# Kernel tuning notes

Hardware: AMD Instinct MI355X
Metric: run time of the kernel (lower is better)

Reference implementation:

```python
import jax, jax.numpy as jnp
import numpy as np

FORGET_BIAS = 1.0  # TF LSTMCell default

def _lstm_step(c, h, x, W, b):
    # TF BasicLSTM/LSTMCell gate order: i, j (cell candidate), f, o
    z = jnp.concatenate([x, h], axis=-1) @ W + b
    i, j, f, o = jnp.split(z, 4, axis=-1)
    c_new = c * jax.nn.sigmoid(f + FORGET_BIAS) + jax.nn.sigmoid(i) * jnp.tanh(j)
    h_new = jnp.tanh(c_new) * jax.nn.sigmoid(o)
    return c_new, h_new

def setup_inputs() -> dict:
    key = jax.random.key(0)
    k1, k2, k3 = jax.random.split(key, 3)
    B, T, D, H1, H2 = 512, 2048, 1, 64, 1
    x = jax.random.normal(k1, (B, T, D), dtype=jnp.float32)
    W1 = jax.random.normal(k2, (D + H1, 4 * H1), dtype=jnp.float32) * 0.1
    b1 = jnp.zeros((4 * H1,), dtype=jnp.float32)
    W2 = jax.random.normal(k3, (H1 + H2, 4 * H2), dtype=jnp.float32) * 0.1
    b2 = jnp.zeros((4 * H2,), dtype=jnp.float32)
    return {"x": x, "W1": W1, "b1": b1, "W2": W2, "b2": b2}

def reference(x, W1, b1, W2, b2):
    B = x.shape[0]
    H1 = W1.shape[1] // 4
    H2 = W2.shape[1] // 4
    init = (jnp.zeros((B, H1), x.dtype), jnp.zeros((B, H1), x.dtype),
            jnp.zeros((B, H2), x.dtype), jnp.zeros((B, H2), x.dtype))

    def step(carry, x_t):
        c1, h1, c2, h2 = carry
        c1, h1 = _lstm_step(c1, h1, x_t, W1, b1)   # layer 1: LSTMCell(64)
        c2, h2 = _lstm_step(c2, h2, h1, W2, b2)    # layer 2: LSTMCell(1)
        return (c1, h1, c2, h2), h2

    xs = jnp.swapaxes(x, 0, 1)           # [T, B, 1]
    _, ys = jax.lax.scan(step, init, xs)  # ys: [T, B, 1]
    return jnp.swapaxes(ys, 0, 1)         # [B, T, 1]
```

## Files before the change

kernel.cpp:

```cpp
#include <hip/hip_runtime.h>

#define TT 2048

typedef float v2f __attribute__((ext_vector_type(2)));
typedef _Float16 h2v __attribute__((ext_vector_type(2)));

__device__ __forceinline__ v2f mk2(float a, float b) { v2f r; r.x = a; r.y = b; return r; }
__device__ __forceinline__ float rcpf(float x) { return __builtin_amdgcn_rcpf(x); }
__device__ __forceinline__ float fsig(float x) { return rcpf(1.0f + __expf(-x)); }
__device__ __forceinline__ float ftanh(float x) {
    return fmaf(2.0f, rcpf(1.0f + __expf(-2.0f * x)), -1.0f);
}

template<int C>
__device__ __forceinline__ float dppmov(float s) {
    return __int_as_float(__builtin_amdgcn_update_dpp(
        __float_as_int(s), __float_as_int(s), C, 0xF, 0xF, false));
}
template<int Q>
__device__ __forceinline__ float qbcast(float x) {
    return __int_as_float(__builtin_amdgcn_update_dpp(
        __float_as_int(x), __float_as_int(x), Q * 0x55, 0xF, 0xF, false));
}

#if __has_builtin(__builtin_amdgcn_fdot2)
#define DOT2(a, b, c) __builtin_amdgcn_fdot2((a), (b), (c), false)
#else
#define DOT2(a, b, c) fmaf((float)(a).x, (float)(b).x, \
                      fmaf((float)(a).y, (float)(b).y, (c)))
#endif

__device__ __forceinline__ h2v pk2(float a, float b) {
#if __has_builtin(__builtin_amdgcn_cvt_pkrtz)
    return __builtin_bit_cast(h2v, __builtin_amdgcn_cvt_pkrtz(a, b));
#else
    h2v r; r.x = (_Float16)a; r.y = (_Float16)b; return r;
#endif
}
__device__ __forceinline__ h2v bch(int v) { return __builtin_bit_cast(h2v, v); }

__global__ __launch_bounds__(64)
__attribute__((amdgpu_waves_per_eu(2, 2)))
void lstm1_f16(const float* __restrict__ x,
               const float* __restrict__ W1,
               const float* __restrict__ b1,
               const float* __restrict__ W2,
               float* __restrict__ zout)
{
    __shared__ __align__(16) float xall[TT];
    __shared__ __align__(16) _Float16 hring[16 * 72];
    __shared__ __align__(16) int wF4[8][64][4];
    __shared__ __align__(16) int wO4[8][64][4];
    __shared__ __align__(16) _Float16 w2lds[4][72];

    const int lane = threadIdx.x & 63;
    const int e    = blockIdx.x;
    const int u    = lane;

    for (int i = lane; i < TT; i += 64) xall[i] = x[(size_t)e * TT + i];
    for (int i = lane; i < 576; i += 64) ((int*)hring)[i] = 0;
    for (int kp = 0; kp < 32; ++kp) {
        wF4[kp >> 2][u][kp & 3] = __builtin_bit_cast(int,
            pk2(W1[(1 + 2*kp)*256 + 128 + u], W1[(2 + 2*kp)*256 + 128 + u]));
        wO4[kp >> 2][u][kp & 3] = __builtin_bit_cast(int,
            pk2(W1[(1 + 2*kp)*256 + 192 + u], W1[(2 + 2*kp)*256 + 192 + u]));
    }
    w2lds[0][lane] = (_Float16)W2[lane * 4 + 0];
    w2lds[1][lane] = (_Float16)W2[lane * 4 + 1];
    w2lds[2][lane] = (_Float16)W2[lane * 4 + 2];
    w2lds[3][lane] = (_Float16)W2[lane * 4 + 3];

#define DWQ(G, GO, q) \
    const h2v w##G##q##x = pk2(W1[(1+8*(q))*256 + (GO)*64 + u], W1[(2+8*(q))*256 + (GO)*64 + u]); \
    const h2v w##G##q##y = pk2(W1[(3+8*(q))*256 + (GO)*64 + u], W1[(4+8*(q))*256 + (GO)*64 + u]); \
    const h2v w##G##q##z = pk2(W1[(5+8*(q))*256 + (GO)*64 + u], W1[(6+8*(q))*256 + (GO)*64 + u]); \
    const h2v w##G##q##w = pk2(W1[(7+8*(q))*256 + (GO)*64 + u], W1[(8+8*(q))*256 + (GO)*64 + u]);
    DWQ(I, 0, 0) DWQ(I, 0, 1) DWQ(I, 0, 2) DWQ(I, 0, 3)
    DWQ(I, 0, 4) DWQ(I, 0, 5) DWQ(I, 0, 6) DWQ(I, 0, 7)
    DWQ(J, 1, 0) DWQ(J, 1, 1) DWQ(J, 1, 2) DWQ(J, 1, 3)
    DWQ(J, 1, 4) DWQ(J, 1, 5) DWQ(J, 1, 6) DWQ(J, 1, 7)
#undef DWQ

    const float w0I = W1[u],        bI = b1[u];
    const float w0J = W1[64 + u],   bJ = b1[64 + u];
    const float w0F = W1[128 + u],  bF = b1[128 + u] + 1.0f;
    const float w0O = W1[192 + u],  bO = b1[192 + u];

    const int tl = lane >> 2, gq = lane & 3;

    float c1 = 0.0f;
    __syncthreads();

    float* __restrict__ zb = zout + (size_t)e * TT * 4;
    const int* __restrict__ wFb = &wF4[0][0][0] + (u << 2);
    const int* __restrict__ wOb = &wO4[0][0][0] + (u << 2);

#define DGIJ(S, q, v) \
    accI##S = DOT2(bch((v).x), wI##q##x, accI##S); \
    accJ##S = DOT2(bch((v).x), wJ##q##x, accJ##S); \
    accI##S = DOT2(bch((v).y), wI##q##y, accI##S); \
    accJ##S = DOT2(bch((v).y), wJ##q##y, accJ##S); \
    accI##S = DOT2(bch((v).z), wI##q##z, accI##S); \
    accJ##S = DOT2(bch((v).z), wJ##q##z, accJ##S); \
    accI##S = DOT2(bch((v).w), wI##q##w, accI##S); \
    accJ##S = DOT2(bch((v).w), wJ##q##w, accJ##S);
#define FOD4(S, g, qv) { \
    const int4 wf_ = *(const int4*)(wFb + (g) * 256); \
    const int4 wo_ = *(const int4*)(wOb + (g) * 256); \
    accF##S = DOT2(bch((qv).x), bch(wf_.x), accF##S); \
    accO##S = DOT2(bch((qv).x), bch(wo_.x), accO##S); \
    accF##S = DOT2(bch((qv).y), bch(wf_.y), accF##S); \
    accO##S = DOT2(bch((qv).y), bch(wo_.y), accO##S); \
    accF##S = DOT2(bch((qv).z), bch(wf_.z), accF##S); \
    accO##S = DOT2(bch((qv).z), bch(wo_.z), accO##S); \
    accF##S = DOT2(bch((qv).w), bch(wf_.w), accF##S); \
    accO##S = DOT2(bch((qv).w), bch(wo_.w), accO##S); \
}

    for (int t = 0; t < TT; ++t) {
        const int4* hp = (const int4*)&hring[((t - 1) & 15) * 72];
        const int4 q0 = hp[0], q1 = hp[1], q2 = hp[2], q3 = hp[3];
        const int4 q4 = hp[4], q5 = hp[5], q6 = hp[6], q7 = hp[7];
        float accI0 = bI, accJ0 = bJ, accF0 = bF, accO0 = bO;
        float accI1 = 0.f, accJ1 = 0.f, accF1 = 0.f, accO1 = 0.f;
        DGIJ(0, 0, q0) DGIJ(1, 4, q4)
        DGIJ(0, 1, q1) DGIJ(1, 5, q5)
        DGIJ(0, 2, q2) DGIJ(1, 6, q6)
        DGIJ(0, 3, q3) DGIJ(1, 7, q7)
        FOD4(0, 0, q0) FOD4(1, 4, q4)
        FOD4(0, 1, q1) FOD4(1, 5, q5)
        FOD4(0, 2, q2) FOD4(1, 6, q6)
        FOD4(0, 3, q3) FOD4(1, 7, q7)
        const float xt = xall[t];
        const float zI = fmaf(xt, w0I, accI0 + accI1);
        const float zJ = fmaf(xt, w0J, accJ0 + accJ1);
        const float zF = fmaf(xt, w0F, accF0 + accF1);
        const float zO = fmaf(xt, w0O, accO0 + accO1);
        const float i_ = fsig(zI);
        const float j_ = ftanh(zJ);
        const float f_ = fsig(zF);
        const float o_ = fsig(zO);
        c1 = fmaf(c1, f_, i_ * j_);
        const float h1 = ftanh(c1) * o_;
        hring[(t & 15) * 72 + u] = (_Float16)h1;

        if ((t & 15) == 15) {
            const int4* hb  = (const int4*)&hring[tl * 72];
            const int4* w2q = (const int4*)&w2lds[gq][0];
            float z2 = 0.0f;
#pragma unroll
            for (int q = 0; q < 8; ++q) {
                const int4 wv = w2q[q];
                const int4 va = hb[q];
                z2 = DOT2(bch(va.x), bch(wv.x), z2);
                z2 = DOT2(bch(va.y), bch(wv.y), z2);
                z2 = DOT2(bch(va.z), bch(wv.z), z2);
                z2 = DOT2(bch(va.w), bch(wv.w), z2);
            }
            zb[(size_t)(t - 15 + tl) * 4 + gq] = z2;
        }
    }
#undef DGIJ
#undef FOD4
}

__global__ __launch_bounds__(64)
void lstm2_chain(const float* __restrict__ zp,
                 const float* __restrict__ W2,
                 const float* __restrict__ b2,
                 float* __restrict__ out)
{
    const int lane = threadIdx.x & 63;
    const int e    = lane >> 2;
    const int g    = lane & 3;
    const int elem = (blockIdx.x << 4) + e;

    const float w2h = W2[256 + g];
    const float bb  = b2[g] + ((g == 2) ? 1.0f : 0.0f);
    const float nlm = (g == 1) ? -2.0f : -1.0f;
    const float k2  = (g == 1) ?  2.0f :  1.0f;
    const float k3  = (g == 1) ? -1.0f :  0.0f;

    const float* __restrict__ zrow = zp + (size_t)elem * TT * 4 + g;
    float* __restrict__ orow = out + (size_t)elem * TT;

    float c2 = 0.0f, h2 = 0.0f;

    float zc[16];
#pragma unroll
    for (int k = 0; k < 16; ++k) zc[k] = zrow[k << 2];

    for (int t0 = 0; t0 < TT; t0 += 16) {
        float zn[16];
        if (t0 + 16 < TT) {
#pragma unroll
            for (int k = 0; k < 16; ++k) zn[k] = zrow[((t0 + 16 + k) << 2)];
        }
        float st0 = 0.f, st1 = 0.f, st2 = 0.f, st3 = 0.f;
#pragma unroll
        for (int k = 0; k < 16; ++k) {
            const float arg = fmaf(w2h, h2, zc[k] + bb);
            const float ev  = __expf(arg * nlm);
            const float rv  = rcpf(1.0f + ev);
            const float v   = fmaf(k2, rv, k3);
            const float vi = qbcast<0>(v), vj = qbcast<1>(v);
            const float vf = qbcast<2>(v), vo = qbcast<3>(v);
            c2 = fmaf(c2, vf, vi * vj);
            h2 = ftanh(c2) * vo;
            const bool mine = (g == (k & 3));
            if ((k >> 2) == 0) st0 = mine ? h2 : st0;
            else if ((k >> 2) == 1) st1 = mine ? h2 : st1;
            else if ((k >> 2) == 2) st2 = mine ? h2 : st2;
            else st3 = mine ? h2 : st3;
        }
        orow[t0 + g]      = st0;
        orow[t0 + 4 + g]  = st1;
        orow[t0 + 8 + g]  = st2;
        orow[t0 + 12 + g] = st3;
#pragma unroll
        for (int k = 0; k < 16; ++k) zc[k] = zn[k];
    }
}

__global__ __launch_bounds__(512)
__attribute__((amdgpu_waves_per_eu(4, 4)))
void lstm2_mono(const float* __restrict__ x,
                const float* __restrict__ W1,
                const float* __restrict__ b1,
                const float* __restrict__ W2,
                const float* __restrict__ b2,
                float* __restrict__ out)
{
    __shared__ __align__(16) float xall[TT + 4];
    __shared__ __align__(16) float h1x[2][80];
    __shared__ __align__(16) float zpq[4][4];
    __shared__ __align__(16) float h2buf[2][64];

    const int tid  = threadIdx.x;
    const int wave = tid >> 6;
    const int lane = tid & 63;
    const int b    = blockIdx.x;

    for (int i = tid; i < TT; i += 512) xall[i] = x[b * TT + i];
    if (tid < 4) xall[TT + tid] = 0.0f;

    const int u    = lane >> 3;
    const int h    = (lane >> 2) & 1;
    const int g    = lane & 3;
    const int unit = (wave << 3) + u;
    const int col  = (g << 6) + unit;

#define DECLW(k) const v2f wq##k = mk2(W1[(1 + 32*h + 2*(k)) * 256 + col], \
                                       W1[(2 + 32*h + 2*(k)) * 256 + col]);
    DECLW(0)  DECLW(1)  DECLW(2)  DECLW(3)
    DECLW(4)  DECLW(5)  DECLW(6)  DECLW(7)
    DECLW(8)  DECLW(9)  DECLW(10) DECLW(11)
    DECLW(12) DECLW(13) DECLW(14) DECLW(15)
#undef DECLW

    const float w0x   = (h == 0) ? W1[col] : 0.0f;
    const float biasF = (h == 0) ? (b1[col] + ((g == 2) ? 1.0f : 0.0f)) : 0.0f;
    const float nlm   = (g == 1) ? -2.0f : -1.0f;
    const bool  isj   = (g == 1);

    const float w2g  = W2[lane * 4 + (wave & 3)];
    const float w2h0 = W2[256], w2h1 = W2[257], w2h2 = W2[258], w2h3 = W2[259];
    const float b20 = b2[0], b21 = b2[1], b22 = b2[2], b23 = b2[3];

    float c1 = 0.0f;
    float c2 = 0.0f, h2v2 = 0.0f;

    const int hbase = h * 48;
    const int ridx  = lane + ((lane >> 5) << 4);
    const int widx  = (unit < 32) ? unit : unit + 16;

    if (tid < 160) ((float*)h1x)[tid] = 0.0f;
    __syncthreads();

    float* __restrict__ outb = out + b * TT;

#define WSUM(s) ({ float _s = (s);                                            \
    _s += dppmov<0x111>(_s); _s += dppmov<0x112>(_s); _s += dppmov<0x114>(_s);\
    _s += dppmov<0x118>(_s); _s += dppmov<0x142>(_s); _s += dppmov<0x143>(_s);\
    _s; })

#define STEP(P, t, xv)                                                        \
    {                                                                         \
        if ((t) < TT) {                                                       \
            const float4* hp = (const float4*)&h1x[P][hbase];                 \
            const float4 q0 = hp[0], q1 = hp[1], q2 = hp[2], q3 = hp[3];      \
            const float4 q4 = hp[4], q5 = hp[5], q6 = hp[6], q7 = hp[7];      \
            v2f a0 = mk2(fmaf((xv), w0x, biasF), 0.0f);                       \
            v2f a1 = mk2(0.f, 0.f), a2 = mk2(0.f, 0.f), a3 = mk2(0.f, 0.f);  \
            a0 = __builtin_elementwise_fma(mk2(q0.x, q0.y), wq0,  a0);        \
            a1 = __builtin_elementwise_fma(mk2(q0.z, q0.w), wq1,  a1);        \
            a2 = __builtin_elementwise_fma(mk2(q1.x, q1.y), wq2,  a2);        \
            a3 = __builtin_elementwise_fma(mk2(q1.z, q1.w), wq3,  a3);        \
            a0 = __builtin_elementwise_fma(mk2(q2.x, q2.y), wq4,  a0);        \
            a1 = __builtin_elementwise_fma(mk2(q2.z, q2.w), wq5,  a1);        \
            a2 = __builtin_elementwise_fma(mk2(q3.x, q3.y), wq6,  a2);        \
            a3 = __builtin_elementwise_fma(mk2(q3.z, q3.w), wq7,  a3);        \
            a0 = __builtin_elementwise_fma(mk2(q4.x, q4.y), wq8,  a0);        \
            a1 = __builtin_elementwise_fma(mk2(q4.z, q4.w), wq9,  a1);        \
            a2 = __builtin_elementwise_fma(mk2(q5.x, q5.y), wq10, a2);        \
            a3 = __builtin_elementwise_fma(mk2(q5.z, q5.w), wq11, a3);        \
            a0 = __builtin_elementwise_fma(mk2(q6.x, q6.y), wq12, a0);        \
            a1 = __builtin_elementwise_fma(mk2(q6.z, q6.w), wq13, a1);        \
            a2 = __builtin_elementwise_fma(mk2(q7.x, q7.y), wq14, a2);        \
            a3 = __builtin_elementwise_fma(mk2(q7.z, q7.w), wq15, a3);        \
            const v2f sv = (a0 + a1) + (a2 + a3);                             \
            const float zh = sv.x + sv.y;                                     \
            const float tshr = dppmov<0x114>(zh);                             \
            const float tshl = dppmov<0x104>(zh);                             \
            const float zfull = zh + (h ? tshr : tshl);                       \
            const float e = __expf(zfull * nlm);                              \
            const float r = rcpf(1.0f + e);                                   \
            const float v = isj ? fmaf(2.0f, r, -1.0f) : r;                   \
            const float gi = qbcast<0>(v), gj = qbcast<1>(v);                 \
            const float gf = qbcast<2>(v), go = qbcast<3>(v);                 \
            c1 = fmaf(c1, gf, gi * gj);                                       \
            const float h1v = ftanh(c1) * go;                                 \
            if ((lane & 7) == 0) h1x[(P) ^ 1][widx] = h1v;                    \
        }                                                                     \
        if (wave < 4 && (t) >= 1 && (t) <= TT) {                              \
            const float s = WSUM(h1x[P][ridx] * w2g);                         \
            if (lane == 63) zpq[((t) - 1) & 3][wave] = s;                     \
        }                                                                     \
        if (wave == 7 && lane == 0 && (t) >= 2 && (t) <= TT + 1) {            \
            const int st = (t) - 2;                                           \
            const float4 z4 = *(const float4*)zpq[st & 3];                    \
            const float zi = z4.x + fmaf(h2v2, w2h0, b20);                    \
            const float zj = z4.y + fmaf(h2v2, w2h1, b21);                    \
            const float zf = z4.z + fmaf(h2v2, w2h2, b22);                    \
            const float zo = z4.w + fmaf(h2v2, w2h3, b23);                    \
            c2 = c2 * fsig(zf + 1.0f) + fsig(zi) * ftanh(zj);                 \
            h2v2 = ftanh(c2) * fsig(zo);                                      \
            h2buf[(st >> 6) & 1][st & 63] = h2v2;                             \
        }                                                                     \
        __syncthreads();                                                      \
        if (wave == 4 && (t) >= 66 && ((t) & 63) == 2) {                      \
            const int blk = ((t) - 66) >> 6;                                  \
            outb[(blk << 6) + lane] = h2buf[blk & 1][lane];                   \
        }                                                                     \
    }

    for (int it = 0; it <= TT + 2; it += 2) {
        const float2 x2 = *(const float2*)&xall[it];
        STEP(0, it,     x2.x)
        STEP(1, it + 1, x2.y)
    }
#undef STEP
#undef WSUM
}

extern "C" void kernel_launch(void* const* d_in, const int* in_sizes, int n_in,
                              void* d_out, int out_size, void* d_ws, size_t ws_size,
                              hipStream_t stream)
{
    const float* x  = (const float*)d_in[0];
    const float* W1 = (const float*)d_in[1];
    const float* b1 = (const float*)d_in[2];
    const float* W2 = (const float*)d_in[3];
    const float* b2 = (const float*)d_in[4];
    float* out = (float*)d_out;

    const size_t need = (size_t)512 * TT * 4 * sizeof(float);
    if (ws_size >= need) {
        float* zp = (float*)d_ws;
        lstm1_f16<<<512, 64, 0, stream>>>(x, W1, b1, W2, zp);
        lstm2_chain<<<512 / 16, 64, 0, stream>>>(zp, W2, b2, out);
    } else {
        lstm2_mono<<<512, 512, 0, stream>>>(x, W1, b1, W2, b2, out);
    }
}
```

Before: 1.051 ms.

## Process two batch elements per wave, sharing LDS-resident weights across both

The layer-1 LSTM kernel now runs two independent batch sequences per 64-lane block, launching 256 blocks instead of 512. All four gate weight sets move from registers or LDS into a single LDS array, and each weight load is reused for both sequences. The aim is to halve weight-load traffic per sequence and give two independent dependency chains to hide latency inside one wave. The cost is double the LDS footprint and more accumulator registers, and waves_per_eu drops to 1.

```diff
diff --git a/kernel.cpp b/kernel.cpp
--- a/kernel.cpp
+++ b/kernel.cpp
@@ -40,47 +40,43 @@
 __device__ __forceinline__ h2v bch(int v) { return __builtin_bit_cast(h2v, v); }
 
 __global__ __launch_bounds__(64)
-__attribute__((amdgpu_waves_per_eu(2, 2)))
-void lstm1_f16(const float* __restrict__ x,
-               const float* __restrict__ W1,
-               const float* __restrict__ b1,
-               const float* __restrict__ W2,
-               float* __restrict__ zout)
+__attribute__((amdgpu_waves_per_eu(1, 1)))
+void lstm1_f16x2(const float* __restrict__ x,
+                 const float* __restrict__ W1,
+                 const float* __restrict__ b1,
+                 const float* __restrict__ W2,
+                 float* __restrict__ zout)
 {
-    __shared__ __align__(16) float xall[TT];
-    __shared__ __align__(16) _Float16 hring[16 * 72];
-    __shared__ __align__(16) int wF4[8][64][4];
-    __shared__ __align__(16) int wO4[8][64][4];
+    __shared__ __align__(16) float xallA[TT];
+    __shared__ __align__(16) float xallB[TT];
+    __shared__ __align__(16) _Float16 hringA[16 * 72];
+    __shared__ __align__(16) _Float16 hringB[16 * 72];
+    __shared__ __align__(16) int wG4[4][8][64][4];
     __shared__ __align__(16) _Float16 w2lds[4][72];
 
     const int lane = threadIdx.x & 63;
-    const int e    = blockIdx.x;
     const int u    = lane;
-
-    for (int i = lane; i < TT; i += 64) xall[i] = x[(size_t)e * TT + i];
-    for (int i = lane; i < 576; i += 64) ((int*)hring)[i] = 0;
-    for (int kp = 0; kp < 32; ++kp) {
-        wF4[kp >> 2][u][kp & 3] = __builtin_bit_cast(int,
-            pk2(W1[(1 + 2*kp)*256 + 128 + u], W1[(2 + 2*kp)*256 + 128 + u]));
-        wO4[kp >> 2][u][kp & 3] = __builtin_bit_cast(int,
-            pk2(W1[(1 + 2*kp)*256 + 192 + u], W1[(2 + 2*kp)*256 + 192 + u]));
-    }
+    const int e0   = blockIdx.x * 2;
+    const int e1   = e0 + 1;
+
+    for (int i = lane; i < TT; i += 64) {
+        xallA[i] = x[(size_t)e0 * TT + i];
+        xallB[i] = x[(size_t)e1 * TT + i];
+    }
+    for (int i = lane; i < 576; i += 64) {
+        ((int*)hringA)[i] = 0;
+        ((int*)hringB)[i] = 0;
+    }
+    for (int g = 0; g < 4; ++g)
+        for (int kp = 0; kp < 32; ++kp)
+            wG4[g][kp >> 2][u][kp & 3] = __builtin_bit_cast(int,
+                pk2(W1[(1 + 2*kp)*256 + g*64 + u],
+                    W1[(2 + 2*kp)*256 + g*64 + u]));
     w2lds[0][lane] = (_Float16)W2[lane * 4 + 0];
     w2lds[1][lane] = (_Float16)W2[lane * 4 + 1];
     w2lds[2][lane] = (_Float16)W2[lane * 4 + 2];
     w2lds[3][lane] = (_Float16)W2[lane * 4 + 3];
 
-#define DWQ(G, GO, q) \
-    const h2v w##G##q##x = pk2(W1[(1+8*(q))*256 + (GO)*64 + u], W1[(2+8*(q))*256 + (GO)*64 + u]); \
-    const h2v w##G##q##y = pk2(W1[(3+8*(q))*256 + (GO)*64 + u], W1[(4+8*(q))*256 + (GO)*64 + u]); \
-    const h2v w##G##q##z = pk2(W1[(5+8*(q))*256 + (GO)*64 + u], W1[(6+8*(q))*256 + (GO)*64 + u]); \
-    const h2v w##G##q##w = pk2(W1[(7+8*(q))*256 + (GO)*64 + u], W1[(8+8*(q))*256 + (GO)*64 + u]);
-    DWQ(I, 0, 0) DWQ(I, 0, 1) DWQ(I, 0, 2) DWQ(I, 0, 3)
-    DWQ(I, 0, 4) DWQ(I, 0, 5) DWQ(I, 0, 6) DWQ(I, 0, 7)
-    DWQ(J, 1, 0) DWQ(J, 1, 1) DWQ(J, 1, 2) DWQ(J, 1, 3)
-    DWQ(J, 1, 4) DWQ(J, 1, 5) DWQ(J, 1, 6) DWQ(J, 1, 7)
-#undef DWQ
-
     const float w0I = W1[u],        bI = b1[u];
     const float w0J = W1[64 + u],   bJ = b1[64 + u];
     const float w0F = W1[128 + u],  bF = b1[128 + u] + 1.0f;
@@ -88,80 +84,116 @@
 
     const int tl = lane >> 2, gq = lane & 3;
 
-    float c1 = 0.0f;
+    float c1A = 0.0f, c1B = 0.0f;
     __syncthreads();
 
-    float* __restrict__ zb = zout + (size_t)e * TT * 4;
-    const int* __restrict__ wFb = &wF4[0][0][0] + (u << 2);
-    const int* __restrict__ wOb = &wO4[0][0][0] + (u << 2);
-
-#define DGIJ(S, q, v) \
-    accI##S = DOT2(bch((v).x), wI##q##x, accI##S); \
-    accJ##S = DOT2(bch((v).x), wJ##q##x, accJ##S); \
-    accI##S = DOT2(bch((v).y), wI##q##y, accI##S); \
-    accJ##S = DOT2(bch((v).y), wJ##q##y, accJ##S); \
-    accI##S = DOT2(bch((v).z), wI##q##z, accI##S); \
-    accJ##S = DOT2(bch((v).z), wJ##q##z, accJ##S); \
-    accI##S = DOT2(bch((v).w), wI##q##w, accI##S); \
-    accJ##S = DOT2(bch((v).w), wJ##q##w, accJ##S);
-#define FOD4(S, g, qv) { \
-    const int4 wf_ = *(const int4*)(wFb + (g) * 256); \
-    const int4 wo_ = *(const int4*)(wOb + (g) * 256); \
-    accF##S = DOT2(bch((qv).x), bch(wf_.x), accF##S); \
-    accO##S = DOT2(bch((qv).x), bch(wo_.x), accO##S); \
-    accF##S = DOT2(bch((qv).y), bch(wf_.y), accF##S); \
-    accO##S = DOT2(bch((qv).y), bch(wo_.y), accO##S); \
-    accF##S = DOT2(bch((qv).z), bch(wf_.z), accF##S); \
-    accO##S = DOT2(bch((qv).z), bch(wo_.z), accO##S); \
-    accF##S = DOT2(bch((qv).w), bch(wf_.w), accF##S); \
-    accO##S = DOT2(bch((qv).w), bch(wo_.w), accO##S); \
+    float* __restrict__ zbA = zout + (size_t)e0 * TT * 4;
+    float* __restrict__ zbB = zout + (size_t)e1 * TT * 4;
+    const int* __restrict__ wIb = &wG4[0][0][0][0] + (u << 2);
+    const int* __restrict__ wJb = &wG4[1][0][0][0] + (u << 2);
+    const int* __restrict__ wFb = &wG4[2][0][0][0] + (u << 2);
+    const int* __restrict__ wOb = &wG4[3][0][0][0] + (u << 2);
+
+#define GDOT(S, g, qa, qb) { \
+    const int4 wi_ = *(const int4*)(wIb + off + (g) * 256); \
+    const int4 wj_ = *(const int4*)(wJb + off + (g) * 256); \
+    const int4 wf_ = *(const int4*)(wFb + off + (g) * 256); \
+    const int4 wo_ = *(const int4*)(wOb + off + (g) * 256); \
+    accIA##S = DOT2(bch((qa).x), bch(wi_.x), accIA##S); \
+    accJA##S = DOT2(bch((qa).x), bch(wj_.x), accJA##S); \
+    accFA##S = DOT2(bch((qa).x), bch(wf_.x), accFA##S); \
+    accOA##S = DOT2(bch((qa).x), bch(wo_.x), accOA##S); \
+    accIB##S = DOT2(bch((qb).x), bch(wi_.x), accIB##S); \
+    accJB##S = DOT2(bch((qb).x), bch(wj_.x), accJB##S); \
+    accFB##S = DOT2(bch((qb).x), bch(wf_.x), accFB##S); \
+    accOB##S = DOT2(bch((qb).x), bch(wo_.x), accOB##S); \
+    accIA##S = DOT2(bch((qa).y), bch(wi_.y), accIA##S); \
+    accJA##S = DOT2(bch((qa).y), bch(wj_.y), accJA##S); \
+    accFA##S = DOT2(bch((qa).y), bch(wf_.y), accFA##S); \
+    accOA##S = DOT2(bch((qa).y), bch(wo_.y), accOA##S); \
+    accIB##S = DOT2(bch((qb).y), bch(wi_.y), accIB##S); \
+    accJB##S = DOT2(bch((qb).y), bch(wj_.y), accJB##S); \
+    accFB##S = DOT2(bch((qb).y), bch(wf_.y), accFB##S); \
+    accOB##S = DOT2(bch((qb).y), bch(wo_.y), accOB##S); \
+    accIA##S = DOT2(bch((qa).z), bch(wi_.z), accIA##S); \
+    accJA##S = DOT2(bch((qa).z), bch(wj_.z), accJA##S); \
+    accFA##S = DOT2(bch((qa).z), bch(wf_.z), accFA##S); \
+    accOA##S = DOT2(bch((qa).z), bch(wo_.z), accOA##S); \
+    accIB##S = DOT2(bch((qb).z), bch(wi_.z), accIB##S); \
+    accJB##S = DOT2(bch((qb).z), bch(wj_.z), accJB##S); \
+    accFB##S = DOT2(bch((qb).z), bch(wf_.z), accFB##S); \
+    accOB##S = DOT2(bch((qb).z), bch(wo_.z), accOB##S); \
+    accIA##S = DOT2(bch((qa).w), bch(wi_.w), accIA##S); \
+    accJA##S = DOT2(bch((qa).w), bch(wj_.w), accJA##S); \
+    accFA##S = DOT2(bch((qa).w), bch(wf_.w), accFA##S); \
+    accOA##S = DOT2(bch((qa).w), bch(wo_.w), accOA##S); \
+    accIB##S = DOT2(bch((qb).w), bch(wi_.w), accIB##S); \
+    accJB##S = DOT2(bch((qb).w), bch(wj_.w), accJB##S); \
+    accFB##S = DOT2(bch((qb).w), bch(wf_.w), accFB##S); \
+    accOB##S = DOT2(bch((qb).w), bch(wo_.w), accOB##S); \
 }
 
     for (int t = 0; t < TT; ++t) {
-        const int4* hp = (const int4*)&hring[((t - 1) & 15) * 72];
-        const int4 q0 = hp[0], q1 = hp[1], q2 = hp[2], q3 = hp[3];
-        const int4 q4 = hp[4], q5 = hp[5], q6 = hp[6], q7 = hp[7];
-        float accI0 = bI, accJ0 = bJ, accF0 = bF, accO0 = bO;
-        float accI1 = 0.f, accJ1 = 0.f, accF1 = 0.f, accO1 = 0.f;
-        DGIJ(0, 0, q0) DGIJ(1, 4, q4)
-        DGIJ(0, 1, q1) DGIJ(1, 5, q5)
-        DGIJ(0, 2, q2) DGIJ(1, 6, q6)
-        DGIJ(0, 3, q3) DGIJ(1, 7, q7)
-        FOD4(0, 0, q0) FOD4(1, 4, q4)
-        FOD4(0, 1, q1) FOD4(1, 5, q5)
-        FOD4(0, 2, q2) FOD4(1, 6, q6)
-        FOD4(0, 3, q3) FOD4(1, 7, q7)
-        const float xt = xall[t];
-        const float zI = fmaf(xt, w0I, accI0 + accI1);
-        const float zJ = fmaf(xt, w0J, accJ0 + accJ1);
-        const float zF = fmaf(xt, w0F, accF0 + accF1);
-        const float zO = fmaf(xt, w0O, accO0 + accO1);
-        const float i_ = fsig(zI);
-        const float j_ = ftanh(zJ);
-        const float f_ = fsig(zF);
-        const float o_ = fsig(zO);
-        c1 = fmaf(c1, f_, i_ * j_);
-        const float h1 = ftanh(c1) * o_;
-        hring[(t & 15) * 72 + u] = (_Float16)h1;
+        int off = 0; asm volatile("" : "+v"(off));
+        const int4* hpA = (const int4*)&hringA[((t - 1) & 15) * 72];
+        const int4* hpB = (const int4*)&hringB[((t - 1) & 15) * 72];
+        const int4 a0 = hpA[0], a1 = hpA[1], a2 = hpA[2], a3 = hpA[3];
+        const int4 a4 = hpA[4], a5 = hpA[5], a6 = hpA[6], a7 = hpA[7];
+        const int4 b0 = hpB[0], b1q = hpB[1], b2q = hpB[2], b3q = hpB[3];
+        const int4 b4 = hpB[4], b5q = hpB[5], b6q = hpB[6], b7q = hpB[7];
+        float accIA0 = bI, accJA0 = bJ, accFA0 = bF, accOA0 = bO;
+        float accIA1 = 0.f, accJA1 = 0.f, accFA1 = 0.f, accOA1 = 0.f;
+        float accIB0 = bI, accJB0 = bJ, accFB0 = bF, accOB0 = bO;
+        float accIB1 = 0.f, accJB1 = 0.f, accFB1 = 0.f, accOB1 = 0.f;
+        GDOT(0, 0, a0, b0)  GDOT(1, 4, a4, b4)
+        GDOT(0, 1, a1, b1q) GDOT(1, 5, a5, b5q)
+        GDOT(0, 2, a2, b2q) GDOT(1, 6, a6, b6q)
+        GDOT(0, 3, a3, b3q) GDOT(1, 7, a7, b7q)
+        const float xtA = xallA[t];
+        const float xtB = xallB[t];
+        const float zIA = fmaf(xtA, w0I, accIA0 + accIA1);
+        const float zJA = fmaf(xtA, w0J, accJA0 + accJA1);
+        const float zFA = fmaf(xtA, w0F, accFA0 + accFA1);
+        const float zOA = fmaf(xtA, w0O, accOA0 + accOA1);
+        const float zIB = fmaf(xtB, w0I, accIB0 + accIB1);
+        const float zJB = fmaf(xtB, w0J, accJB0 + accJB1);
+        const float zFB = fmaf(xtB, w0F, accFB0 + accFB1);
+        const float zOB = fmaf(xtB, w0O, accOB0 + accOB1);
+        const float iA = fsig(zIA),  iB = fsig(zIB);
+        const float jA = ftanh(zJA), jB = ftanh(zJB);
+        const float fA = fsig(zFA),  fB = fsig(zFB);
+        const float oA = fsig(zOA),  oB = fsig(zOB);
+        c1A = fmaf(c1A, fA, iA * jA);
+        c1B = fmaf(c1B, fB, iB * jB);
+        const float h1A = ftanh(c1A) * oA;
+        const float h1B = ftanh(c1B) * oB;
+        hringA[(t & 15) * 72 + u] = (_Float16)h1A;
+        hringB[(t & 15) * 72 + u] = (_Float16)h1B;
 
         if ((t & 15) == 15) {
-            const int4* hb  = (const int4*)&hring[tl * 72];
             const int4* w2q = (const int4*)&w2lds[gq][0];
-            float z2 = 0.0f;
+            const int4* hbA = (const int4*)&hringA[tl * 72];
+            const int4* hbB = (const int4*)&hringB[tl * 72];
+            float z2A = 0.0f, z2B = 0.0f;
 #pragma unroll
             for (int q = 0; q < 8; ++q) {
                 const int4 wv = w2q[q];
-                const int4 va = hb[q];
-                z2 = DOT2(bch(va.x), bch(wv.x), z2);
-                z2 = DOT2(bch(va.y), bch(wv.y), z2);
-                z2 = DOT2(bch(va.z), bch(wv.z), z2);
-                z2 = DOT2(bch(va.w), bch(wv.w), z2);
+                const int4 va = hbA[q];
+                const int4 vb = hbB[q];
+                z2A = DOT2(bch(va.x), bch(wv.x), z2A);
+                z2A = DOT2(bch(va.y), bch(wv.y), z2A);
+                z2A = DOT2(bch(va.z), bch(wv.z), z2A);
+                z2A = DOT2(bch(va.w), bch(wv.w), z2A);
+                z2B = DOT2(bch(vb.x), bch(wv.x), z2B);
+                z2B = DOT2(bch(vb.y), bch(wv.y), z2B);
+                z2B = DOT2(bch(vb.z), bch(wv.z), z2B);
+                z2B = DOT2(bch(vb.w), bch(wv.w), z2B);
             }
-            zb[(size_t)(t - 15 + tl) * 4 + gq] = z2;
+            zbA[(size_t)(t - 15 + tl) * 4 + gq] = z2A;
+            zbB[(size_t)(t - 15 + tl) * 4 + gq] = z2B;
         }
     }
-#undef DGIJ
-#undef FOD4
+#undef GDOT
 }
 
 __global__ __launch_bounds__(64)
@@ -367,7 +399,7 @@
     const size_t need = (size_t)512 * TT * 4 * sizeof(float);
     if (ws_size >= need) {
         float* zp = (float*)d_ws;
-        lstm1_f16<<<512, 64, 0, stream>>>(x, W1, b1, W2, zp);
+        lstm1_f16x2<<<256, 64, 0, stream>>>(x, W1, b1, W2, zp);
         lstm2_chain<<<512 / 16, 64, 0, stream>>>(zp, W2, b2, out);
     } else {
         lstm2_mono<<<512, 512, 0, stream>>>(x, W1, b1, W2, b2, out);
```

Result: slower. 2.026 ms (+92.7%).

## Split layer-1 LSTM recurrence reduction across two waves with LDS partial exchange

Applied to the files above, without the earlier changes.

Layer-1 kernel now uses 128 threads per sequence. Each wave handles half of the hidden-state reduction dimension and keeps all four gates' weights in registers, replacing the LDS weight reads for the f and o gates. Partial gate sums are exchanged through double-buffered shared memory with a block barrier every timestep. This halves the per-wave dot-product chain but adds a barrier per step, and the hring update relies on implicit ordering between the two waves.

```diff
diff --git a/kernel.cpp b/kernel.cpp
--- a/kernel.cpp
+++ b/kernel.cpp
@@ -39,9 +39,9 @@
 }
 __device__ __forceinline__ h2v bch(int v) { return __builtin_bit_cast(h2v, v); }
 
-__global__ __launch_bounds__(64)
-__attribute__((amdgpu_waves_per_eu(2, 2)))
-void lstm1_f16(const float* __restrict__ x,
+__global__ __launch_bounds__(128)
+__attribute__((amdgpu_waves_per_eu(1)))
+void lstm1_ks2(const float* __restrict__ x,
                const float* __restrict__ W1,
                const float* __restrict__ b1,
                const float* __restrict__ W2,
@@ -49,119 +49,112 @@
 {
     __shared__ __align__(16) float xall[TT];
     __shared__ __align__(16) _Float16 hring[16 * 72];
-    __shared__ __align__(16) int wF4[8][64][4];
-    __shared__ __align__(16) int wO4[8][64][4];
+    __shared__ __align__(16) float4 pex[2][2][64];
     __shared__ __align__(16) _Float16 w2lds[4][72];
 
-    const int lane = threadIdx.x & 63;
+    const int tid  = threadIdx.x;
+    const int w    = tid >> 6;
+    const int u    = tid & 63;
     const int e    = blockIdx.x;
-    const int u    = lane;
-
-    for (int i = lane; i < TT; i += 64) xall[i] = x[(size_t)e * TT + i];
-    for (int i = lane; i < 576; i += 64) ((int*)hring)[i] = 0;
-    for (int kp = 0; kp < 32; ++kp) {
-        wF4[kp >> 2][u][kp & 3] = __builtin_bit_cast(int,
-            pk2(W1[(1 + 2*kp)*256 + 128 + u], W1[(2 + 2*kp)*256 + 128 + u]));
-        wO4[kp >> 2][u][kp & 3] = __builtin_bit_cast(int,
-            pk2(W1[(1 + 2*kp)*256 + 192 + u], W1[(2 + 2*kp)*256 + 192 + u]));
-    }
-    w2lds[0][lane] = (_Float16)W2[lane * 4 + 0];
-    w2lds[1][lane] = (_Float16)W2[lane * 4 + 1];
-    w2lds[2][lane] = (_Float16)W2[lane * 4 + 2];
-    w2lds[3][lane] = (_Float16)W2[lane * 4 + 3];
+    const int kbase = w << 4;
+
+    for (int i = tid; i < TT; i += 128) xall[i] = x[(size_t)e * TT + i];
+    for (int i = tid; i < 576; i += 128) ((int*)hring)[i] = 0;
+    if (tid < 64) {
+        w2lds[0][u] = (_Float16)W2[u * 4 + 0];
+        w2lds[1][u] = (_Float16)W2[u * 4 + 1];
+        w2lds[2][u] = (_Float16)W2[u * 4 + 2];
+        w2lds[3][u] = (_Float16)W2[u * 4 + 3];
+    }
 
 #define DWQ(G, GO, q) \
-    const h2v w##G##q##x = pk2(W1[(1+8*(q))*256 + (GO)*64 + u], W1[(2+8*(q))*256 + (GO)*64 + u]); \
-    const h2v w##G##q##y = pk2(W1[(3+8*(q))*256 + (GO)*64 + u], W1[(4+8*(q))*256 + (GO)*64 + u]); \
-    const h2v w##G##q##z = pk2(W1[(5+8*(q))*256 + (GO)*64 + u], W1[(6+8*(q))*256 + (GO)*64 + u]); \
-    const h2v w##G##q##w = pk2(W1[(7+8*(q))*256 + (GO)*64 + u], W1[(8+8*(q))*256 + (GO)*64 + u]);
+    const h2v w##G##q##x = pk2(W1[(1+2*(kbase+4*(q)+0))*256 + (GO)*64 + u], \
+                               W1[(2+2*(kbase+4*(q)+0))*256 + (GO)*64 + u]); \
+    const h2v w##G##q##y = pk2(W1[(1+2*(kbase+4*(q)+1))*256 + (GO)*64 + u], \
+                               W1[(2+2*(kbase+4*(q)+1))*256 + (GO)*64 + u]); \
+    const h2v w##G##q##z = pk2(W1[(1+2*(kbase+4*(q)+2))*256 + (GO)*64 + u], \
+                               W1[(2+2*(kbase+4*(q)+2))*256 + (GO)*64 + u]); \
+    const h2v w##G##q##w = pk2(W1[(1+2*(kbase+4*(q)+3))*256 + (GO)*64 + u], \
+                               W1[(2+2*(kbase+4*(q)+3))*256 + (GO)*64 + u]);
     DWQ(I, 0, 0) DWQ(I, 0, 1) DWQ(I, 0, 2) DWQ(I, 0, 3)
-    DWQ(I, 0, 4) DWQ(I, 0, 5) DWQ(I, 0, 6) DWQ(I, 0, 7)
     DWQ(J, 1, 0) DWQ(J, 1, 1) DWQ(J, 1, 2) DWQ(J, 1, 3)
-    DWQ(J, 1, 4) DWQ(J, 1, 5) DWQ(J, 1, 6) DWQ(J, 1, 7)
+    DWQ(F, 2, 0) DWQ(F, 2, 1) DWQ(F, 2, 2) DWQ(F, 2, 3)
+    DWQ(O, 3, 0) DWQ(O, 3, 1) DWQ(O, 3, 2) DWQ(O, 3, 3)
 #undef DWQ
 
-    const float w0I = W1[u],        bI = b1[u];
-    const float w0J = W1[64 + u],   bJ = b1[64 + u];
-    const float w0F = W1[128 + u],  bF = b1[128 + u] + 1.0f;
-    const float w0O = W1[192 + u],  bO = b1[192 + u];
-
-    const int tl = lane >> 2, gq = lane & 3;
+    const float w0I = W1[u];
+    const float w0J = W1[64 + u];
+    const float w0F = W1[128 + u];
+    const float w0O = W1[192 + u];
+    const float aI = (w == 0) ? b1[u]              : 0.0f;
+    const float aJ = (w == 0) ? b1[64 + u]         : 0.0f;
+    const float aF = (w == 0) ? (b1[128 + u] + 1.0f) : 0.0f;
+    const float aO = (w == 0) ? b1[192 + u]        : 0.0f;
+
+    const int tl = u >> 2, gq = u & 3;
 
     float c1 = 0.0f;
     __syncthreads();
 
     float* __restrict__ zb = zout + (size_t)e * TT * 4;
-    const int* __restrict__ wFb = &wF4[0][0][0] + (u << 2);
-    const int* __restrict__ wOb = &wO4[0][0][0] + (u << 2);
-
-#define DGIJ(S, q, v) \
-    accI##S = DOT2(bch((v).x), wI##q##x, accI##S); \
-    accJ##S = DOT2(bch((v).x), wJ##q##x, accJ##S); \
-    accI##S = DOT2(bch((v).y), wI##q##y, accI##S); \
-    accJ##S = DOT2(bch((v).y), wJ##q##y, accJ##S); \
-    accI##S = DOT2(bch((v).z), wI##q##z, accI##S); \
-    accJ##S = DOT2(bch((v).z), wJ##q##z, accJ##S); \
-    accI##S = DOT2(bch((v).w), wI##q##w, accI##S); \
-    accJ##S = DOT2(bch((v).w), wJ##q##w, accJ##S);
-#define FOD4(S, g, qv) { \
-    const int4 wf_ = *(const int4*)(wFb + (g) * 256); \
-    const int4 wo_ = *(const int4*)(wOb + (g) * 256); \
-    accF##S = DOT2(bch((qv).x), bch(wf_.x), accF##S); \
-    accO##S = DOT2(bch((qv).x), bch(wo_.x), accO##S); \
-    accF##S = DOT2(bch((qv).y), bch(wf_.y), accF##S); \
-    accO##S = DOT2(bch((qv).y), bch(wo_.y), accO##S); \
-    accF##S = DOT2(bch((qv).z), bch(wf_.z), accF##S); \
-    accO##S = DOT2(bch((qv).z), bch(wo_.z), accO##S); \
-    accF##S = DOT2(bch((qv).w), bch(wf_.w), accF##S); \
-    accO##S = DOT2(bch((qv).w), bch(wo_.w), accO##S); \
-}
+
+#define DG(acc, WQ, qv) \
+    acc = DOT2(bch((qv).x), WQ##x, acc); \
+    acc = DOT2(bch((qv).y), WQ##y, acc); \
+    acc = DOT2(bch((qv).z), WQ##z, acc); \
+    acc = DOT2(bch((qv).w), WQ##w, acc);
 
     for (int t = 0; t < TT; ++t) {
         const int4* hp = (const int4*)&hring[((t - 1) & 15) * 72];
-        const int4 q0 = hp[0], q1 = hp[1], q2 = hp[2], q3 = hp[3];
-        const int4 q4 = hp[4], q5 = hp[5], q6 = hp[6], q7 = hp[7];
-        float accI0 = bI, accJ0 = bJ, accF0 = bF, accO0 = bO;
+        const int4 q0 = hp[(w << 2) + 0], q1 = hp[(w << 2) + 1];
+        const int4 q2 = hp[(w << 2) + 2], q3 = hp[(w << 2) + 3];
+        float accI0 = aI, accJ0 = aJ, accF0 = aF, accO0 = aO;
         float accI1 = 0.f, accJ1 = 0.f, accF1 = 0.f, accO1 = 0.f;
-        DGIJ(0, 0, q0) DGIJ(1, 4, q4)
-        DGIJ(0, 1, q1) DGIJ(1, 5, q5)
-        DGIJ(0, 2, q2) DGIJ(1, 6, q6)
-        DGIJ(0, 3, q3) DGIJ(1, 7, q7)
-        FOD4(0, 0, q0) FOD4(1, 4, q4)
-        FOD4(0, 1, q1) FOD4(1, 5, q5)
-        FOD4(0, 2, q2) FOD4(1, 6, q6)
-        FOD4(0, 3, q3) FOD4(1, 7, q7)
+        DG(accI0, wI0, q0) DG(accJ0, wJ0, q0) DG(accF0, wF0, q0) DG(accO0, wO0, q0)
+        DG(accI0, wI1, q1) DG(accJ0, wJ1, q1) DG(accF0, wF1, q1) DG(accO0, wO1, q1)
+        DG(accI1, wI2, q2) DG(accJ1, wJ2, q2) DG(accF1, wF2, q2) DG(accO1, wO2, q2)
+        DG(accI1, wI3, q3) DG(accJ1, wJ3, q3) DG(accF1, wF3, q3) DG(accO1, wO3, q3)
+        const float mI = accI0 + accI1;
+        const float mJ = accJ0 + accJ1;
+        const float mF = accF0 + accF1;
+        const float mO = accO0 + accO1;
+        pex[t & 1][w][u] = make_float4(mI, mJ, mF, mO);
+        __syncthreads();
+        const float4 po = pex[t & 1][w ^ 1][u];
         const float xt = xall[t];
-        const float zI = fmaf(xt, w0I, accI0 + accI1);
-        const float zJ = fmaf(xt, w0J, accJ0 + accJ1);
-        const float zF = fmaf(xt, w0F, accF0 + accF1);
-        const float zO = fmaf(xt, w0O, accO0 + accO1);
+        const float zI = fmaf(xt, w0I, mI + po.x);
+        const float zJ = fmaf(xt, w0J, mJ + po.y);
+        const float zF = fmaf(xt, w0F, mF + po.z);
+        const float zO = fmaf(xt, w0O, mO + po.w);
         const float i_ = fsig(zI);
         const float j_ = ftanh(zJ);
         const float f_ = fsig(zF);
         const float o_ = fsig(zO);
         c1 = fmaf(c1, f_, i_ * j_);
         const float h1 = ftanh(c1) * o_;
-        hring[(t & 15) * 72 + u] = (_Float16)h1;
+        if ((u >> 5) == w) hring[(t & 15) * 72 + u] = (_Float16)h1;
 
         if ((t & 15) == 15) {
-            const int4* hb  = (const int4*)&hring[tl * 72];
-            const int4* w2q = (const int4*)&w2lds[gq][0];
-            float z2 = 0.0f;
-#pragma unroll
-            for (int q = 0; q < 8; ++q) {
-                const int4 wv = w2q[q];
-                const int4 va = hb[q];
-                z2 = DOT2(bch(va.x), bch(wv.x), z2);
-                z2 = DOT2(bch(va.y), bch(wv.y), z2);
-                z2 = DOT2(bch(va.z), bch(wv.z), z2);
-                z2 = DOT2(bch(va.w), bch(wv.w), z2);
+            __syncthreads();
+            if (w == 0) {
+                const int4* hb  = (const int4*)&hring[tl * 72];
+                const int4* w2q = (const int4*)&w2lds[gq][0];
+                float z2 = 0.0f;
+#pragma unroll
+                for (int q = 0; q < 8; ++q) {
+                    const int4 wv = w2q[q];
+                    const int4 va = hb[q];
+                    z2 = DOT2(bch(va.x), bch(wv.x), z2);
+                    z2 = DOT2(bch(va.y), bch(wv.y), z2);
+                    z2 = DOT2(bch(va.z), bch(wv.z), z2);
+                    z2 = DOT2(bch(va.w), bch(wv.w), z2);
+                }
+                zb[(size_t)(t - 15 + tl) * 4 + gq] = z2;
             }
-            zb[(size_t)(t - 15 + tl) * 4 + gq] = z2;
+            __syncthreads();
         }
     }
-#undef DGIJ
-#undef FOD4
+#undef DG
 }
 
 __global__ __launch_bounds__(64)
@@ -367,7 +360,7 @@
     const size_t need = (size_t)512 * TT * 4 * sizeof(float);
     if (ws_size >= need) {
         float* zp = (float*)d_ws;
-        lstm1_f16<<<512, 64, 0, stream>>>(x, W1, b1, W2, zp);
+        lstm1_ks2<<<512, 128, 0, stream>>>(x, W1, b1, W2, zp);
         lstm2_chain<<<512 / 16, 64, 0, stream>>>(zp, W2, b2, out);
     } else {
         lstm2_mono<<<512, 512, 0, stream>>>(x, W1, b1, W2, b2, out);
```

After: 1.488 ms. 41.6% more time.

## Compute layer-1 recurrent matvec with 16x16x32 f16 MFMA instead of dot2

Applied to the files above, without the earlier changes.

Replaces the per-lane packed-f16 dot2 recurrent matvec for all four gates with 32 MFMA 16x16x32 f16 instructions per timestep. The previous hidden state is broadcast as the A operand, and the weights are held as B fragments in registers. The goal is to move the dominant per-step VALU and LDS weight-read work onto the matrix cores and drop the LDS-resident F/O weight tables. The price is redundant MFMA rows, since all 16 rows carry the same h. It also adds a serial MFMA latency chain on every step of the recurrence, plus a lane-dependent selection to pull each unit's gate value out of the accumulators.

```diff
diff --git a/kernel.cpp b/kernel.cpp
--- a/kernel.cpp
+++ b/kernel.cpp
@@ -4,6 +4,8 @@
 
 typedef float v2f __attribute__((ext_vector_type(2)));
 typedef _Float16 h2v __attribute__((ext_vector_type(2)));
+typedef _Float16 f16x8 __attribute__((ext_vector_type(8)));
+typedef float f32x4 __attribute__((ext_vector_type(4)));
 
 __device__ __forceinline__ v2f mk2(float a, float b) { v2f r; r.x = a; r.y = b; return r; }
 __device__ __forceinline__ float rcpf(float x) { return __builtin_amdgcn_rcpf(x); }
@@ -30,56 +32,47 @@
                       fmaf((float)(a).y, (float)(b).y, (c)))
 #endif
 
-__device__ __forceinline__ h2v pk2(float a, float b) {
-#if __has_builtin(__builtin_amdgcn_cvt_pkrtz)
-    return __builtin_bit_cast(h2v, __builtin_amdgcn_cvt_pkrtz(a, b));
-#else
-    h2v r; r.x = (_Float16)a; r.y = (_Float16)b; return r;
-#endif
-}
 __device__ __forceinline__ h2v bch(int v) { return __builtin_bit_cast(h2v, v); }
 
 __global__ __launch_bounds__(64)
-__attribute__((amdgpu_waves_per_eu(2, 2)))
-void lstm1_f16(const float* __restrict__ x,
-               const float* __restrict__ W1,
-               const float* __restrict__ b1,
-               const float* __restrict__ W2,
-               float* __restrict__ zout)
+__attribute__((amdgpu_waves_per_eu(1)))
+void lstm1_mfma(const float* __restrict__ x,
+                const float* __restrict__ W1,
+                const float* __restrict__ b1,
+                const float* __restrict__ W2,
+                float* __restrict__ zout)
 {
     __shared__ __align__(16) float xall[TT];
     __shared__ __align__(16) _Float16 hring[16 * 72];
-    __shared__ __align__(16) int wF4[8][64][4];
-    __shared__ __align__(16) int wO4[8][64][4];
     __shared__ __align__(16) _Float16 w2lds[4][72];
 
     const int lane = threadIdx.x & 63;
     const int e    = blockIdx.x;
     const int u    = lane;
+    const int lg   = lane >> 4;
+    const int j16  = lane & 15;
 
     for (int i = lane; i < TT; i += 64) xall[i] = x[(size_t)e * TT + i];
     for (int i = lane; i < 576; i += 64) ((int*)hring)[i] = 0;
-    for (int kp = 0; kp < 32; ++kp) {
-        wF4[kp >> 2][u][kp & 3] = __builtin_bit_cast(int,
-            pk2(W1[(1 + 2*kp)*256 + 128 + u], W1[(2 + 2*kp)*256 + 128 + u]));
-        wO4[kp >> 2][u][kp & 3] = __builtin_bit_cast(int,
-            pk2(W1[(1 + 2*kp)*256 + 192 + u], W1[(2 + 2*kp)*256 + 192 + u]));
-    }
     w2lds[0][lane] = (_Float16)W2[lane * 4 + 0];
     w2lds[1][lane] = (_Float16)W2[lane * 4 + 1];
     w2lds[2][lane] = (_Float16)W2[lane * 4 + 2];
     w2lds[3][lane] = (_Float16)W2[lane * 4 + 3];
 
-#define DWQ(G, GO, q) \
-    const h2v w##G##q##x = pk2(W1[(1+8*(q))*256 + (GO)*64 + u], W1[(2+8*(q))*256 + (GO)*64 + u]); \
-    const h2v w##G##q##y = pk2(W1[(3+8*(q))*256 + (GO)*64 + u], W1[(4+8*(q))*256 + (GO)*64 + u]); \
-    const h2v w##G##q##z = pk2(W1[(5+8*(q))*256 + (GO)*64 + u], W1[(6+8*(q))*256 + (GO)*64 + u]); \
-    const h2v w##G##q##w = pk2(W1[(7+8*(q))*256 + (GO)*64 + u], W1[(8+8*(q))*256 + (GO)*64 + u]);
-    DWQ(I, 0, 0) DWQ(I, 0, 1) DWQ(I, 0, 2) DWQ(I, 0, 3)
-    DWQ(I, 0, 4) DWQ(I, 0, 5) DWQ(I, 0, 6) DWQ(I, 0, 7)
-    DWQ(J, 1, 0) DWQ(J, 1, 1) DWQ(J, 1, 2) DWQ(J, 1, 3)
-    DWQ(J, 1, 4) DWQ(J, 1, 5) DWQ(J, 1, 6) DWQ(J, 1, 7)
-#undef DWQ
+#define MKB(kt, n) ({ f16x8 f_; \
+    _Pragma("unroll") \
+    for (int j = 0; j < 8; ++j) \
+        f_[j] = (_Float16)W1[(size_t)(1 + (kt)*32 + lg*8 + j) * 256 + 16*(n) + j16]; \
+    f_; })
+    const f16x8 wB0_0  = MKB(0,0),  wB0_1  = MKB(0,1),  wB0_2  = MKB(0,2),  wB0_3  = MKB(0,3);
+    const f16x8 wB0_4  = MKB(0,4),  wB0_5  = MKB(0,5),  wB0_6  = MKB(0,6),  wB0_7  = MKB(0,7);
+    const f16x8 wB0_8  = MKB(0,8),  wB0_9  = MKB(0,9),  wB0_10 = MKB(0,10), wB0_11 = MKB(0,11);
+    const f16x8 wB0_12 = MKB(0,12), wB0_13 = MKB(0,13), wB0_14 = MKB(0,14), wB0_15 = MKB(0,15);
+    const f16x8 wB1_0  = MKB(1,0),  wB1_1  = MKB(1,1),  wB1_2  = MKB(1,2),  wB1_3  = MKB(1,3);
+    const f16x8 wB1_4  = MKB(1,4),  wB1_5  = MKB(1,5),  wB1_6  = MKB(1,6),  wB1_7  = MKB(1,7);
+    const f16x8 wB1_8  = MKB(1,8),  wB1_9  = MKB(1,9),  wB1_10 = MKB(1,10), wB1_11 = MKB(1,11);
+    const f16x8 wB1_12 = MKB(1,12), wB1_13 = MKB(1,13), wB1_14 = MKB(1,14), wB1_15 = MKB(1,15);
+#undef MKB
 
     const float w0I = W1[u],        bI = b1[u];
     const float w0J = W1[64 + u],   bJ = b1[64 + u];
@@ -92,50 +85,28 @@
     __syncthreads();
 
     float* __restrict__ zb = zout + (size_t)e * TT * 4;
-    const int* __restrict__ wFb = &wF4[0][0][0] + (u << 2);
-    const int* __restrict__ wOb = &wO4[0][0][0] + (u << 2);
-
-#define DGIJ(S, q, v) \
-    accI##S = DOT2(bch((v).x), wI##q##x, accI##S); \
-    accJ##S = DOT2(bch((v).x), wJ##q##x, accJ##S); \
-    accI##S = DOT2(bch((v).y), wI##q##y, accI##S); \
-    accJ##S = DOT2(bch((v).y), wJ##q##y, accJ##S); \
-    accI##S = DOT2(bch((v).z), wI##q##z, accI##S); \
-    accJ##S = DOT2(bch((v).z), wJ##q##z, accJ##S); \
-    accI##S = DOT2(bch((v).w), wI##q##w, accI##S); \
-    accJ##S = DOT2(bch((v).w), wJ##q##w, accJ##S);
-#define FOD4(S, g, qv) { \
-    const int4 wf_ = *(const int4*)(wFb + (g) * 256); \
-    const int4 wo_ = *(const int4*)(wOb + (g) * 256); \
-    accF##S = DOT2(bch((qv).x), bch(wf_.x), accF##S); \
-    accO##S = DOT2(bch((qv).x), bch(wo_.x), accO##S); \
-    accF##S = DOT2(bch((qv).y), bch(wf_.y), accF##S); \
-    accO##S = DOT2(bch((qv).y), bch(wo_.y), accO##S); \
-    accF##S = DOT2(bch((qv).z), bch(wf_.z), accF##S); \
-    accO##S = DOT2(bch((qv).z), bch(wo_.z), accO##S); \
-    accF##S = DOT2(bch((qv).w), bch(wf_.w), accF##S); \
-    accO##S = DOT2(bch((qv).w), bch(wo_.w), accO##S); \
-}
+    const f32x4 zf = {0.0f, 0.0f, 0.0f, 0.0f};
+
+#define MM(a, b, c) __builtin_amdgcn_mfma_f32_16x16x32_f16((a), (b), (c), 0, 0, 0)
+#define TACC(n) const f32x4 ac##n = MM(A1, wB1_##n, MM(A0, wB0_##n, zf));
 
     for (int t = 0; t < TT; ++t) {
-        const int4* hp = (const int4*)&hring[((t - 1) & 15) * 72];
-        const int4 q0 = hp[0], q1 = hp[1], q2 = hp[2], q3 = hp[3];
-        const int4 q4 = hp[4], q5 = hp[5], q6 = hp[6], q7 = hp[7];
-        float accI0 = bI, accJ0 = bJ, accF0 = bF, accO0 = bO;
-        float accI1 = 0.f, accJ1 = 0.f, accF1 = 0.f, accO1 = 0.f;
-        DGIJ(0, 0, q0) DGIJ(1, 4, q4)
-        DGIJ(0, 1, q1) DGIJ(1, 5, q5)
-        DGIJ(0, 2, q2) DGIJ(1, 6, q6)
-        DGIJ(0, 3, q3) DGIJ(1, 7, q7)
-        FOD4(0, 0, q0) FOD4(1, 4, q4)
-        FOD4(0, 1, q1) FOD4(1, 5, q5)
-        FOD4(0, 2, q2) FOD4(1, 6, q6)
-        FOD4(0, 3, q3) FOD4(1, 7, q7)
+        const int slot = ((t - 1) & 15) * 72;
+        const f16x8 A0 = *(const f16x8*)&hring[slot + lg * 8];
+        const f16x8 A1 = *(const f16x8*)&hring[slot + 32 + lg * 8];
+        TACC(0)  TACC(1)  TACC(2)  TACC(3)
+        TACC(4)  TACC(5)  TACC(6)  TACC(7)
+        TACC(8)  TACC(9)  TACC(10) TACC(11)
+        TACC(12) TACC(13) TACC(14) TACC(15)
+        const float zIs = (lg == 0) ? ac0.x  : (lg == 1) ? ac1.x  : (lg == 2) ? ac2.x  : ac3.x;
+        const float zJs = (lg == 0) ? ac4.x  : (lg == 1) ? ac5.x  : (lg == 2) ? ac6.x  : ac7.x;
+        const float zFs = (lg == 0) ? ac8.x  : (lg == 1) ? ac9.x  : (lg == 2) ? ac10.x : ac11.x;
+        const float zOs = (lg == 0) ? ac12.x : (lg == 1) ? ac13.x : (lg == 2) ? ac14.x : ac15.x;
         const float xt = xall[t];
-        const float zI = fmaf(xt, w0I, accI0 + accI1);
-        const float zJ = fmaf(xt, w0J, accJ0 + accJ1);
-        const float zF = fmaf(xt, w0F, accF0 + accF1);
-        const float zO = fmaf(xt, w0O, accO0 + accO1);
+        const float zI = fmaf(xt, w0I, zIs + bI);
+        const float zJ = fmaf(xt, w0J, zJs + bJ);
+        const float zF = fmaf(xt, w0F, zFs + bF);
+        const float zO = fmaf(xt, w0O, zOs + bO);
         const float i_ = fsig(zI);
         const float j_ = ftanh(zJ);
         const float f_ = fsig(zF);
@@ -160,8 +131,8 @@
             zb[(size_t)(t - 15 + tl) * 4 + gq] = z2;
         }
     }
-#undef DGIJ
-#undef FOD4
+#undef TACC
+#undef MM
 }
 
 __global__ __launch_bounds__(64)
@@ -367,7 +338,7 @@
     const size_t need = (size_t)512 * TT * 4 * sizeof(float);
     if (ws_size >= need) {
         float* zp = (float*)d_ws;
-        lstm1_f16<<<512, 64, 0, stream>>>(x, W1, b1, W2, zp);
+        lstm1_mfma<<<512, 64, 0, stream>>>(x, W1, b1, W2, zp);
         lstm2_chain<<<512 / 16, 64, 0, stream>>>(zp, W2, b2, out);
     } else {
         lstm2_mono<<<512, 512, 0, stream>>>(x, W1, b1, W2, b2, out);
```

Result: slower. 1.411 ms (+34.2%).
